# Kernel optimization log

Measured on AMD Instinct MI355X. Metric: run time of the kernel, lower is better.

## Reference

```python
import jax, jax.numpy as jnp
import numpy as np

N = 100000
E = 1600000
IN_C, HID_C, OUT_C = 64, 64, 32


def setup_inputs() -> dict:
    key = jax.random.key(0)
    ks = jax.random.split(key, 8)
    x = jax.random.normal(ks[0], (N, IN_C), dtype=jnp.float32)
    edge_index = jax.random.randint(ks[1], (2, E), 0, N, dtype=jnp.int64)
    # GCNConv weights (glorot-ish scale) and biases
    W1 = jax.random.normal(ks[2], (IN_C, HID_C), dtype=jnp.float32) / np.sqrt(IN_C)
    b1 = jnp.zeros((HID_C,), dtype=jnp.float32)
    W2 = jax.random.normal(ks[3], (HID_C, HID_C), dtype=jnp.float32) / np.sqrt(HID_C)
    b2 = jnp.zeros((HID_C,), dtype=jnp.float32)
    Wlin = jax.random.normal(ks[4], (HID_C, OUT_C), dtype=jnp.float32) / np.sqrt(HID_C)
    blin = jnp.zeros((OUT_C,), dtype=jnp.float32)
    return {"x": x, "edge_index": edge_index, "W1": W1, "b1": b1,
            "W2": W2, "b2": b2, "Wlin": Wlin, "blin": blin}


def _gcn_norm(edge_index):
    # PyG GCNConv default: add self-loops, symmetric normalization.
    loop = jnp.arange(N, dtype=edge_index.dtype)
    row = jnp.concatenate([edge_index[0], loop])  # source nodes [E+N]
    col = jnp.concatenate([edge_index[1], loop])  # target nodes [E+N]
    deg = jax.ops.segment_sum(jnp.ones_like(col, dtype=jnp.float32), col,
                              num_segments=N)
    dinv = jnp.where(deg > 0, deg ** -0.5, 0.0)
    norm = dinv[row] * dinv[col]  # [E+N]
    return row, col, norm


def _gcn_conv(h, W, b, row, col, norm):
    h = h @ W                                  # [N, F_out]
    msg = h[row] * norm[:, None]               # gather + scale, [E+N, F_out]
    out = jax.ops.segment_sum(msg, col, num_segments=N)  # scatter-add
    return out + b


def reference(x, edge_index, W1, b1, W2, b2, Wlin, blin):
    row, col, norm = _gcn_norm(edge_index)
    h = jax.nn.relu(_gcn_conv(x, W1, b1, row, col, norm))
    h = jax.nn.relu(_gcn_conv(h, W2, b2, row, col, norm))
    return h @ Wlin + blin
```

## Files before the change

kernel.cpp:

```cpp
#include <hip/hip_runtime.h>
#include <hip/hip_fp16.h>

#define IN_C 64
#define HID_C 64
#define OUT_C 32
#define S_NODES  512
#define S_CAP  12288
#define CHUNK_E 2048

typedef _Float16 f16_t;
typedef f16_t f16x2 __attribute__((ext_vector_type(2)));

__device__ __forceinline__ float dot2(unsigned int a, unsigned int b, float c) {
#if __has_builtin(__builtin_amdgcn_fdot2)
    return __builtin_amdgcn_fdot2(*(f16x2*)&a, *(f16x2*)&b, c, false);
#else
    float2 af = __half22float2(*(__half2*)&a);
    float2 bf = __half22float2(*(__half2*)&b);
    return fmaf(af.x, bf.x, fmaf(af.y, bf.y, c));
#endif
}

__device__ __forceinline__ int ld_edge(const void* ei, int idx, int is64) {
    if (is64) return (int)((const long long*)ei)[idx];
    return ((const int*)ei)[idx];
}

__global__ __launch_bounds__(256) void fat(const void* ei, int E,
                                           int* bcur, int NB,
                                           int* __restrict__ staging,
                                           int NEB, int GB,
                                           const float* __restrict__ x,
                                           const float* __restrict__ W1,
                                           unsigned short* __restrict__ tbuf, int n,
                                           const float* __restrict__ W2,
                                           const float* __restrict__ Wlin,
                                           unsigned short* __restrict__ Wh2,
                                           unsigned short* __restrict__ Whl) {
    __shared__ __align__(16) int smem[3073];
    int tid = threadIdx.x;
    int b = blockIdx.x;
    if (b < NEB) {
        int* cnt = smem;          int* boff = smem + 256;
        int* lcur = smem + 512;   int* gbase = smem + 768;
        int* stg = smem + 1024;
        int* ps64 = smem + 3072;
        if (tid == 0) *ps64 = 1;
        cnt[tid] = 0;
        __syncthreads();
        if (2 * tid + 1 < 2 * E && ((const int*)ei)[2 * tid + 1] != 0) *ps64 = 0;
        __syncthreads();
        int is64 = *ps64;
        int e0 = b * CHUNK_E;
        int e1 = min(E, e0 + CHUNK_E);
        for (int e = e0 + tid; e < e1; e += 256) {
            int dst = ld_edge(ei, E + e, is64);
            atomicAdd(&cnt[dst >> 9], 1);
        }
        __syncthreads();
        int v = cnt[tid];
        gbase[tid] = v;
        __syncthreads();
        for (int o = 1; o < 256; o <<= 1) {
            int u = (tid >= o) ? gbase[tid - o] : 0;
            __syncthreads();
            gbase[tid] += u;
            __syncthreads();
        }
        boff[tid] = gbase[tid] - v;
        lcur[tid] = boff[tid];
        __syncthreads();
        for (int e = e0 + tid; e < e1; e += 256) {
            int src = ld_edge(ei, e, is64);
            int dst = ld_edge(ei, E + e, is64);
            int p = atomicAdd(&lcur[dst >> 9], 1);
            stg[p] = src | ((dst & 511) << 17);
        }
        __syncthreads();
        if (tid < NB && cnt[tid] > 0) gbase[tid] = atomicAdd(&bcur[tid], cnt[tid]);
        __syncthreads();
        int sw = tid >> 4, sl = tid & 15;
        for (int bk = sw; bk < NB; bk += 16) {
            int c = cnt[bk];
            if (c == 0) continue;
            int o = boff[bk], g = gbase[bk];
            size_t gb = (size_t)bk * S_CAP;
            for (int j = sl; j < c; j += 16) {
                if (g + j < S_CAP) staging[gb + g + j] = stg[o + j];
            }
        }
    } else if (b < NEB + GB) {
        uint4* sA = (uint4*)smem;
        int bb = b - NEB;
        int lane = tid & 63, wave = tid >> 6;
        unsigned int wu[32];
#pragma unroll
        for (int k = 0; k < 32; k++) {
            f16x2 p;
            p.x = (f16_t)W1[(2 * k) * 64 + lane];
            p.y = (f16_t)W1[(2 * k + 1) * 64 + lane];
            wu[k] = *(unsigned int*)&p;
        }
        int base = bb * 32;
        const float2* A2 = (const float2*)x;
        int lim = n * 32;
        for (int i = tid; i < 1024; i += 256) {
            int gi = base * 32 + i;
            float2 v = (gi < lim) ? A2[gi] : make_float2(0.f, 0.f);
            ((__half2*)sA)[i] = __floats2half2_rn(v.x, v.y);
        }
        __syncthreads();
        int r0 = base + wave * 8;
        int r1 = min(r0 + 8, n);
        for (int r = r0; r < r1; r++) {
            int rr = r - base;
            float a0 = 0.f, a1 = 0.f;
#pragma unroll
            for (int j = 0; j < 8; j++) {
                uint4 u = sA[rr * 8 + j];
                a0 = dot2(u.x, wu[4 * j], a0);
                a1 = dot2(u.y, wu[4 * j + 1], a1);
                a0 = dot2(u.z, wu[4 * j + 2], a0);
                a1 = dot2(u.w, wu[4 * j + 3], a1);
            }
            __half hv = __float2half_rn(a0 + a1);
            tbuf[(size_t)r * 64 + lane] = *(unsigned short*)&hv;
        }
    } else {
        for (int i = tid; i < 4096; i += 256) {
            int r = i >> 6, c = i & 63;
            f16_t h2 = (f16_t)W2[r * 64 + c];
            Wh2[c * 64 + r] = *(unsigned short*)&h2;
        }
        for (int i = tid; i < 2048; i += 256) {
            int r = i >> 5, c = i & 31;
            f16_t h = (f16_t)Wlin[r * 32 + c];
            Whl[c * 64 + r] = *(unsigned short*)&h;
        }
    }
}

__global__ __launch_bounds__(256) void place_fine(const int* __restrict__ staging,
                                                  const int* __restrict__ bcur,
                                                  int* __restrict__ offs,
                                                  float* __restrict__ dinv,
                                                  int* __restrict__ rec, int N, int NB) {
    __shared__ int sdeg[S_NODES];
    __shared__ int tsum[256];
    __shared__ int curs[S_NODES];
    __shared__ int sb[256];
    int tid = threadIdx.x;
    int vcnt = (tid < NB) ? min(bcur[tid], S_CAP) : 0;
    sb[tid] = vcnt;
    sdeg[tid] = 0;
    sdeg[tid + 256] = 0;
    __syncthreads();
    for (int o = 1; o < 256; o <<= 1) {
        int u = (tid >= o) ? sb[tid - o] : 0;
        __syncthreads();
        sb[tid] += u;
        __syncthreads();
    }
    int cnt = min(bcur[blockIdx.x], S_CAP);
    int bbase = sb[blockIdx.x] - cnt;
    if (blockIdx.x == NB - 1 && tid == 0) offs[N] = sb[255];
    int base = blockIdx.x * S_NODES;
    int nn = min(S_NODES, N - base);
    size_t sbase = (size_t)blockIdx.x * S_CAP;
    for (int j = tid; j < cnt; j += 256) atomicAdd(&sdeg[staging[sbase + j] >> 17], 1);
    __syncthreads();
    int d0 = sdeg[2 * tid], d1 = sdeg[2 * tid + 1];
    tsum[tid] = d0 + d1;
    __syncthreads();
    for (int o = 1; o < 256; o <<= 1) {
        int v = (tid >= o) ? tsum[tid - o] : 0;
        __syncthreads();
        tsum[tid] += v;
        __syncthreads();
    }
    int pre = bbase + ((tid == 0) ? 0 : tsum[tid - 1]);
    curs[2 * tid] = pre;
    curs[2 * tid + 1] = pre + d0;
    if (2 * tid < nn) {
        offs[base + 2 * tid] = pre;
        dinv[base + 2 * tid] = rsqrtf((float)(d0 + 1));
    }
    if (2 * tid + 1 < nn) {
        offs[base + 2 * tid + 1] = pre + d0;
        dinv[base + 2 * tid + 1] = rsqrtf((float)(d1 + 1));
    }
    __syncthreads();
    for (int j = tid; j < cnt; j += 256) {
        int pk = staging[sbase + j];
        int p = atomicAdd(&curs[pk >> 17], 1);
        rec[p] = pk & 0x1FFFF;
    }
}

template <int WDINV>
__global__ void aggregate(const unsigned short* __restrict__ t,
                          const int* __restrict__ offs, const int* __restrict__ rec,
                          const float* __restrict__ dinv, const float* __restrict__ bias,
                          unsigned short* __restrict__ acc, int n) {
    int wave = (blockIdx.x * blockDim.x + threadIdx.x) >> 6;
    int lane = threadIdx.x & 63;
    if (wave >= n) return;
    int g = lane >> 3;
    int gl = lane & 7;
    int beg = offs[wave], end = offs[wave + 1];
    int m = end - beg + 1;
    const uint4* t4 = (const uint4*)t;
    float s[8] = {0.f, 0.f, 0.f, 0.f, 0.f, 0.f, 0.f, 0.f};
    for (int i = 0; i < m; i += 32) {
        int srcs[4];
        float ws[4];
#pragma unroll
        for (int u = 0; u < 4; u++) {
            int it = i + u * 8 + g;
            srcs[u] = (it == 0) ? wave : ((it < m) ? rec[beg + it - 1] : wave);
            if (WDINV) {
                float dv = dinv[srcs[u]];
                ws[u] = (it < m) ? dv : 0.f;
            } else {
                ws[u] = (it < m) ? 1.f : 0.f;
            }
        }
        uint4 vs[4];
#pragma unroll
        for (int u = 0; u < 4; u++) vs[u] = t4[(size_t)srcs[u] * 8 + gl];
#pragma unroll
        for (int u = 0; u < 4; u++) {
            float w = ws[u];
            float2 f0 = __half22float2(*(__half2*)&vs[u].x);
            float2 f1 = __half22float2(*(__half2*)&vs[u].y);
            float2 f2 = __half22float2(*(__half2*)&vs[u].z);
            float2 f3 = __half22float2(*(__half2*)&vs[u].w);
            s[0] = fmaf(f0.x, w, s[0]);
            s[1] = fmaf(f0.y, w, s[1]);
            s[2] = fmaf(f1.x, w, s[2]);
            s[3] = fmaf(f1.y, w, s[3]);
            s[4] = fmaf(f2.x, w, s[4]);
            s[5] = fmaf(f2.y, w, s[5]);
            s[6] = fmaf(f3.x, w, s[6]);
            s[7] = fmaf(f3.y, w, s[7]);
        }
    }
#pragma unroll
    for (int k = 0; k < 8; k++) {
        s[k] += __shfl_xor(s[k], 8);
        s[k] += __shfl_xor(s[k], 16);
        s[k] += __shfl_xor(s[k], 32);
    }
    if (g == 0) {
        float d = dinv[wave];
        const float4* b4 = (const float4*)bias;
        float4 bb0 = b4[gl * 2], bb1 = b4[gl * 2 + 1];
        float o0 = fmaxf(fmaf(s[0], d, bb0.x), 0.f);
        float o1 = fmaxf(fmaf(s[1], d, bb0.y), 0.f);
        float o2 = fmaxf(fmaf(s[2], d, bb0.z), 0.f);
        float o3 = fmaxf(fmaf(s[3], d, bb0.w), 0.f);
        float o4 = fmaxf(fmaf(s[4], d, bb1.x), 0.f);
        float o5 = fmaxf(fmaf(s[5], d, bb1.y), 0.f);
        float o6 = fmaxf(fmaf(s[6], d, bb1.z), 0.f);
        float o7 = fmaxf(fmaf(s[7], d, bb1.w), 0.f);
        __half2 p0 = __floats2half2_rn(o0, o1);
        __half2 p1 = __floats2half2_rn(o2, o3);
        __half2 p2 = __floats2half2_rn(o4, o5);
        __half2 p3 = __floats2half2_rn(o6, o7);
        ((uint4*)acc)[(size_t)wave * 8 + gl] =
            make_uint4(*(unsigned int*)&p0, *(unsigned int*)&p1,
                       *(unsigned int*)&p2, *(unsigned int*)&p3);
    }
}

__global__ __launch_bounds__(256) void gemm64(const unsigned short* __restrict__ in,
                                              const unsigned short* __restrict__ Wh,
                                              unsigned short* __restrict__ out,
                                              const float* __restrict__ dinv, int n) {
    __shared__ uint4 sA[32 * 8];
    int tid = threadIdx.x;
    int lane = tid & 63, wave = tid >> 6;
    unsigned int wu[32];
    {
        const uint4* col = (const uint4*)(Wh + (size_t)lane * 64);
#pragma unroll
        for (int j = 0; j < 8; j++) {
            uint4 w4 = col[j];
            wu[4 * j] = w4.x; wu[4 * j + 1] = w4.y;
            wu[4 * j + 2] = w4.z; wu[4 * j + 3] = w4.w;
        }
    }
    int base = blockIdx.x * 32;
    const uint2* A2 = (const uint2*)in;
    int lim = n * 16;
    for (int i = tid; i < 512; i += 256) {
        int gi = base * 16 + i;
        ((uint2*)sA)[i] = (gi < lim) ? A2[gi] : make_uint2(0u, 0u);
    }
    __syncthreads();
    int r0 = base + wave * 8;
    int r1 = min(r0 + 8, n);
    for (int r = r0; r < r1; r++) {
        int rr = r - base;
        float a0 = 0.f, a1 = 0.f;
#pragma unroll
        for (int j = 0; j < 8; j++) {
            uint4 u = sA[rr * 8 + j];
            a0 = dot2(u.x, wu[4 * j], a0);
            a1 = dot2(u.y, wu[4 * j + 1], a1);
            a0 = dot2(u.z, wu[4 * j + 2], a0);
            a1 = dot2(u.w, wu[4 * j + 3], a1);
        }
        __half hv = __float2half_rn((a0 + a1) * dinv[r]);
        out[(size_t)r * 64 + lane] = *(unsigned short*)&hv;
    }
}

__global__ __launch_bounds__(256) void gemm32(const unsigned short* __restrict__ in,
                                              const unsigned short* __restrict__ Wh,
                                              const float* __restrict__ b,
                                              float* __restrict__ out, int n) {
    __shared__ uint4 sA[32 * 8];
    int tid = threadIdx.x;
    int lane = tid & 63, wave = tid >> 6;
    int c = lane & 31;
    unsigned int wu[32];
    {
        const uint4* col = (const uint4*)(Wh + (size_t)c * 64);
#pragma unroll
        for (int j = 0; j < 8; j++) {
            uint4 w4 = col[j];
            wu[4 * j] = w4.x; wu[4 * j + 1] = w4.y;
            wu[4 * j + 2] = w4.z; wu[4 * j + 3] = w4.w;
        }
    }
    float bl = b[c];
    int base = blockIdx.x * 32;
    const uint2* A2 = (const uint2*)in;
    int lim = n * 16;
    for (int i = tid; i < 512; i += 256) {
        int gi = base * 16 + i;
        ((uint2*)sA)[i] = (gi < lim) ? A2[gi] : make_uint2(0u, 0u);
    }
    __syncthreads();
    int r0 = base + wave * 8;
    int r1 = min(r0 + 8, n);
    for (int r = r0; r < r1; r++) {
        int rr = r - base;
        float a0 = 0.f, a1 = 0.f;
#pragma unroll
        for (int j = 0; j < 8; j++) {
            uint4 u = sA[rr * 8 + j];
            a0 = dot2(u.x, wu[4 * j], a0);
            a1 = dot2(u.y, wu[4 * j + 1], a1);
            a0 = dot2(u.z, wu[4 * j + 2], a0);
            a1 = dot2(u.w, wu[4 * j + 3], a1);
        }
        if (lane < 32) out[(size_t)r * 32 + c] = bl + a0 + a1;
    }
}

extern "C" void kernel_launch(void* const* d_in, const int* in_sizes, int n_in,
                              void* d_out, int out_size, void* d_ws, size_t ws_size,
                              hipStream_t stream) {
    (void)n_in; (void)out_size; (void)ws_size;
    const float* x    = (const float*)d_in[0];
    const void*  ei   = d_in[1];
    const float* W1   = (const float*)d_in[2];
    const float* b1   = (const float*)d_in[3];
    const float* W2   = (const float*)d_in[4];
    const float* b2   = (const float*)d_in[5];
    const float* Wlin = (const float*)d_in[6];
    const float* blin = (const float*)d_in[7];
    float* out = (float*)d_out;

    const int N = in_sizes[0] / IN_C;
    const int E = in_sizes[1] / 2;
    const int NB = (N + S_NODES - 1) / S_NODES;
    const int NEB = (E + CHUNK_E - 1) / CHUNK_E;
    const int GB = (N + 31) / 32;

    char* ws = (char*)d_ws;
    size_t off = 0;
    auto alloc = [&](size_t bytes) -> void* {
        size_t a = (off + 255) & ~(size_t)255;
        off = a + bytes;
        return (void*)(ws + a);
    };
    int*   offs    = (int*)  alloc((size_t)(N + 1) * 4);
    float* dinv    = (float*)alloc((size_t)N * 4);
    int*   bcur    = (int*)  alloc((size_t)NB * 4);
    int*   rec     = (int*)  alloc((size_t)E * 4);
    int*   staging = (int*)  alloc((size_t)NB * S_CAP * 4);
    unsigned short* tbuf = (unsigned short*)alloc((size_t)N * HID_C * 2);
    unsigned short* acc  = (unsigned short*)alloc((size_t)N * HID_C * 2);
    unsigned short* Wh2  = (unsigned short*)alloc(64 * 64 * 2);
    unsigned short* Whl  = (unsigned short*)alloc(64 * 32 * 2);

    hipMemsetAsync(bcur, 0, (size_t)NB * 4, stream);

    fat<<<NEB + GB + 1, 256, 0, stream>>>(ei, E, bcur, NB, staging, NEB, GB,
                                          x, W1, tbuf, N, W2, Wlin, Wh2, Whl);
    place_fine<<<NB, 256, 0, stream>>>(staging, bcur, offs, dinv, rec, N, NB);

    aggregate<1><<<(N + 3) / 4, 256, 0, stream>>>(tbuf, offs, rec, dinv, b1, acc, N);
    gemm64<<<GB, 256, 0, stream>>>(acc, Wh2, tbuf, dinv, N);
    aggregate<0><<<(N + 3) / 4, 256, 0, stream>>>(tbuf, offs, rec, dinv, b2, acc, N);
    gemm32<<<GB, 256, 0, stream>>>(acc, Whl, blin, out, N);
}
```

Measured before the change: 266.5 us.

## Pre-scale layer-1 features by dinv in place_fine and trim aggregate tail gathers

The first GEMM now writes fp32 features, and place_fine, which already knows the degrees, scales each row by its dinv and converts to fp16. This removes the per-edge dinv gather from the first aggregation, so both aggregations share one unweighted kernel. The aggregate loop also dispatches tail chunks with 1, 2 or 3 unrolled gathers instead of always issuing 4. The cost is an extra fp32 write and read of the N×64 feature buffer, and the conversion pass is serialized inside place_fine.

```diff
diff --git a/kernel.cpp b/kernel.cpp
--- a/kernel.cpp
+++ b/kernel.cpp
@@ -32,7 +32,7 @@
                                            int NEB, int GB,
                                            const float* __restrict__ x,
                                            const float* __restrict__ W1,
-                                           unsigned short* __restrict__ tbuf, int n,
+                                           float* __restrict__ t32, int n,
                                            const float* __restrict__ W2,
                                            const float* __restrict__ Wlin,
                                            unsigned short* __restrict__ Wh2,
@@ -123,8 +123,7 @@
                 a0 = dot2(u.z, wu[4 * j + 2], a0);
                 a1 = dot2(u.w, wu[4 * j + 3], a1);
             }
-            __half hv = __float2half_rn(a0 + a1);
-            tbuf[(size_t)r * 64 + lane] = *(unsigned short*)&hv;
+            t32[(size_t)r * 64 + lane] = a0 + a1;
         }
     } else {
         for (int i = tid; i < 4096; i += 256) {
@@ -144,11 +143,15 @@
                                                   const int* __restrict__ bcur,
                                                   int* __restrict__ offs,
                                                   float* __restrict__ dinv,
-                                                  int* __restrict__ rec, int N, int NB) {
+                                                  int* __restrict__ rec,
+                                                  const float* __restrict__ t32,
+                                                  unsigned short* __restrict__ t16,
+                                                  int N, int NB) {
     __shared__ int sdeg[S_NODES];
     __shared__ int tsum[256];
     __shared__ int curs[S_NODES];
     __shared__ int sb[256];
+    __shared__ float sdinv[S_NODES];
     int tid = threadIdx.x;
     int vcnt = (tid < NB) ? min(bcur[tid], S_CAP) : 0;
     sb[tid] = vcnt;
@@ -181,13 +184,17 @@
     int pre = bbase + ((tid == 0) ? 0 : tsum[tid - 1]);
     curs[2 * tid] = pre;
     curs[2 * tid + 1] = pre + d0;
+    float dv0 = rsqrtf((float)(d0 + 1));
+    float dv1 = rsqrtf((float)(d1 + 1));
+    sdinv[2 * tid] = dv0;
+    sdinv[2 * tid + 1] = dv1;
     if (2 * tid < nn) {
         offs[base + 2 * tid] = pre;
-        dinv[base + 2 * tid] = rsqrtf((float)(d0 + 1));
+        dinv[base + 2 * tid] = dv0;
     }
     if (2 * tid + 1 < nn) {
         offs[base + 2 * tid + 1] = pre + d0;
-        dinv[base + 2 * tid + 1] = rsqrtf((float)(d1 + 1));
+        dinv[base + 2 * tid + 1] = dv1;
     }
     __syncthreads();
     for (int j = tid; j < cnt; j += 256) {
@@ -195,9 +202,53 @@
         int p = atomicAdd(&curs[pk >> 17], 1);
         rec[p] = pk & 0x1FFFF;
     }
-}
-
-template <int WDINV>
+    const float4* tin = (const float4*)t32 + (size_t)base * 16;
+    uint2* tout = (uint2*)t16 + (size_t)base * 16;
+    int jmax = nn * 16;
+    for (int j = tid; j < jmax; j += 256) {
+        float4 v = tin[j];
+        float w = sdinv[j >> 4];
+        __half2 h0 = __floats2half2_rn(v.x * w, v.y * w);
+        __half2 h1 = __floats2half2_rn(v.z * w, v.w * w);
+        tout[j] = make_uint2(*(unsigned int*)&h0, *(unsigned int*)&h1);
+    }
+}
+
+__device__ __forceinline__ void agg_consume(const uint4& v, float w, float s[8]) {
+    float2 f0 = __half22float2(*(__half2*)&v.x);
+    float2 f1 = __half22float2(*(__half2*)&v.y);
+    float2 f2 = __half22float2(*(__half2*)&v.z);
+    float2 f3 = __half22float2(*(__half2*)&v.w);
+    s[0] = fmaf(f0.x, w, s[0]);
+    s[1] = fmaf(f0.y, w, s[1]);
+    s[2] = fmaf(f1.x, w, s[2]);
+    s[3] = fmaf(f1.y, w, s[3]);
+    s[4] = fmaf(f2.x, w, s[4]);
+    s[5] = fmaf(f2.y, w, s[5]);
+    s[6] = fmaf(f3.x, w, s[6]);
+    s[7] = fmaf(f3.y, w, s[7]);
+}
+
+template <int NU>
+__device__ __forceinline__ void agg_chunk(const uint4* __restrict__ t4,
+                                          const int* __restrict__ rec,
+                                          int beg, int node, int m, int i,
+                                          int g, int gl, float s[8]) {
+    int srcs[NU];
+    float ws[NU];
+    uint4 vs[NU];
+#pragma unroll
+    for (int u = 0; u < NU; u++) {
+        int it = i + u * 8 + g;
+        srcs[u] = (it == 0) ? node : ((it < m) ? rec[beg + it - 1] : node);
+        ws[u] = (it < m) ? 1.f : 0.f;
+    }
+#pragma unroll
+    for (int u = 0; u < NU; u++) vs[u] = t4[(size_t)srcs[u] * 8 + gl];
+#pragma unroll
+    for (int u = 0; u < NU; u++) agg_consume(vs[u], ws[u], s);
+}
+
 __global__ void aggregate(const unsigned short* __restrict__ t,
                           const int* __restrict__ offs, const int* __restrict__ rec,
                           const float* __restrict__ dinv, const float* __restrict__ bias,
@@ -211,40 +262,12 @@
     int m = end - beg + 1;
     const uint4* t4 = (const uint4*)t;
     float s[8] = {0.f, 0.f, 0.f, 0.f, 0.f, 0.f, 0.f, 0.f};
-    for (int i = 0; i < m; i += 32) {
-        int srcs[4];
-        float ws[4];
-#pragma unroll
-        for (int u = 0; u < 4; u++) {
-            int it = i + u * 8 + g;
-            srcs[u] = (it == 0) ? wave : ((it < m) ? rec[beg + it - 1] : wave);
-            if (WDINV) {
-                float dv = dinv[srcs[u]];
-                ws[u] = (it < m) ? dv : 0.f;
-            } else {
-                ws[u] = (it < m) ? 1.f : 0.f;
-            }
-        }
-        uint4 vs[4];
-#pragma unroll
-        for (int u = 0; u < 4; u++) vs[u] = t4[(size_t)srcs[u] * 8 + gl];
-#pragma unroll
-        for (int u = 0; u < 4; u++) {
-            float w = ws[u];
-            float2 f0 = __half22float2(*(__half2*)&vs[u].x);
-            float2 f1 = __half22float2(*(__half2*)&vs[u].y);
-            float2 f2 = __half22float2(*(__half2*)&vs[u].z);
-            float2 f3 = __half22float2(*(__half2*)&vs[u].w);
-            s[0] = fmaf(f0.x, w, s[0]);
-            s[1] = fmaf(f0.y, w, s[1]);
-            s[2] = fmaf(f1.x, w, s[2]);
-            s[3] = fmaf(f1.y, w, s[3]);
-            s[4] = fmaf(f2.x, w, s[4]);
-            s[5] = fmaf(f2.y, w, s[5]);
-            s[6] = fmaf(f3.x, w, s[6]);
-            s[7] = fmaf(f3.y, w, s[7]);
-        }
-    }
+    int i = 0;
+    for (; m - i > 24; i += 32) agg_chunk<4>(t4, rec, beg, wave, m, i, g, gl, s);
+    int rem = m - i;
+    if (rem > 16)     agg_chunk<3>(t4, rec, beg, wave, m, i, g, gl, s);
+    else if (rem > 8) agg_chunk<2>(t4, rec, beg, wave, m, i, g, gl, s);
+    else if (rem > 0) agg_chunk<1>(t4, rec, beg, wave, m, i, g, gl, s);
 #pragma unroll
     for (int k = 0; k < 8; k++) {
         s[k] += __shfl_xor(s[k], 8);
@@ -392,19 +415,21 @@
     int*   bcur    = (int*)  alloc((size_t)NB * 4);
     int*   rec     = (int*)  alloc((size_t)E * 4);
     int*   staging = (int*)  alloc((size_t)NB * S_CAP * 4);
-    unsigned short* tbuf = (unsigned short*)alloc((size_t)N * HID_C * 2);
-    unsigned short* acc  = (unsigned short*)alloc((size_t)N * HID_C * 2);
-    unsigned short* Wh2  = (unsigned short*)alloc(64 * 64 * 2);
-    unsigned short* Whl  = (unsigned short*)alloc(64 * 32 * 2);
+    float* t32     = (float*)alloc((size_t)N * HID_C * 4);
+    unsigned short* t16 = (unsigned short*)alloc((size_t)N * HID_C * 2);
+    unsigned short* Wh2 = (unsigned short*)alloc(64 * 64 * 2);
+    unsigned short* Whl = (unsigned short*)alloc(64 * 32 * 2);
+    unsigned short* acc = (unsigned short*)t32;
 
     hipMemsetAsync(bcur, 0, (size_t)NB * 4, stream);
 
     fat<<<NEB + GB + 1, 256, 0, stream>>>(ei, E, bcur, NB, staging, NEB, GB,
-                                          x, W1, tbuf, N, W2, Wlin, Wh2, Whl);
-    place_fine<<<NB, 256, 0, stream>>>(staging, bcur, offs, dinv, rec, N, NB);
-
-    aggregate<1><<<(N + 3) / 4, 256, 0, stream>>>(tbuf, offs, rec, dinv, b1, acc, N);
-    gemm64<<<GB, 256, 0, stream>>>(acc, Wh2, tbuf, dinv, N);
-    aggregate<0><<<(N + 3) / 4, 256, 0, stream>>>(tbuf, offs, rec, dinv, b2, acc, N);
+                                          x, W1, t32, N, W2, Wlin, Wh2, Whl);
+    place_fine<<<NB, 256, 0, stream>>>(staging, bcur, offs, dinv, rec,
+                                       t32, t16, N, NB);
+
+    aggregate<<<(N + 3) / 4, 256, 0, stream>>>(t16, offs, rec, dinv, b1, acc, N);
+    gemm64<<<GB, 256, 0, stream>>>(acc, Wh2, t16, dinv, N);
+    aggregate<<<(N + 3) / 4, 256, 0, stream>>>(t16, offs, rec, dinv, b2, acc, N);
     gemm32<<<GB, 256, 0, stream>>>(acc, Whl, blin, out, N);
 }
```

After: 265.9 us. About the same (-0.2%).
